# Kernel optimization log

Measured on AMD Instinct MI355X. Metric: run time of the kernel, lower is better.

The kernel has to match this reference:

```python
import jax, jax.numpy as jnp
import numpy as np
from jax import lax

B, C_IN, H, W = 4, 256, 64, 64
C_OUT = 512
KEY_DIM = C_OUT // 2   # 256
VAL_DIM = C_OUT // 2   # 256
HEADS = 8
EPS = 1e-5


def _conv(x, w, stride, pad):
    return lax.conv_general_dilated(
        x, w, (stride, stride), [(pad, pad), (pad, pad)],
        dimension_numbers=('NCHW', 'OIHW', 'NCHW'))


def setup_inputs() -> dict:
    key = jax.random.key(0)
    ks = jax.random.split(key, 10)
    x = jax.random.normal(ks[0], (B, C_IN, H, W), jnp.float32)
    bn_gamma = jax.random.uniform(ks[1], (C_IN,), jnp.float32, 0.5, 1.5)
    bn_beta = jax.random.normal(ks[2], (C_IN,), jnp.float32) * 0.1
    bn_mean = jax.random.normal(ks[3], (C_IN,), jnp.float32) * 0.1
    bn_var = jax.random.uniform(ks[4], (C_IN,), jnp.float32, 0.5, 1.5)
    w_short = jax.random.normal(ks[5], (C_OUT, C_IN, 3, 3), jnp.float32) * (1.0 / np.sqrt(C_IN * 9))
    wq = jax.random.normal(ks[6], (KEY_DIM, C_IN, 1, 1), jnp.float32) * (1.0 / np.sqrt(C_IN))
    wk = jax.random.normal(ks[7], (KEY_DIM, C_IN, 1, 1), jnp.float32) * (1.0 / np.sqrt(C_IN))
    wv = jax.random.normal(ks[8], (VAL_DIM, C_IN, 1, 1), jnp.float32) * (1.0 / np.sqrt(C_IN))
    wo = jax.random.normal(ks[9], (C_OUT, VAL_DIM, 1, 1), jnp.float32) * (1.0 / np.sqrt(VAL_DIM))
    return dict(x=x, bn_gamma=bn_gamma, bn_beta=bn_beta, bn_mean=bn_mean,
                bn_var=bn_var, w_short=w_short, wq=wq, wk=wk, wv=wv, wo=wo)


def reference(x, bn_gamma, bn_beta, bn_mean, bn_var, w_short, wq, wk, wv, wo):
    # BatchNorm (inference: running stats) + ReLU, fused elementwise chain
    inv = bn_gamma / jnp.sqrt(bn_var + EPS)
    h = jax.nn.relu((x - bn_mean[None, :, None, None]) * inv[None, :, None, None]
                    + bn_beta[None, :, None, None])

    # Projection shortcut: 3x3 conv, stride 2, pad 1, no bias -> [B, C_OUT, H/2, W/2]
    shortcut = _conv(h, w_short, 2, 1)

    # DOWN attention: queries at stride 2 (downsampled grid), keys/values at full res
    q = _conv(h, wq, 2, 0)   # [B, KEY_DIM, H/2, W/2]
    k = _conv(h, wk, 1, 0)   # [B, KEY_DIM, H, W]
    v = _conv(h, wv, 1, 0)   # [B, VAL_DIM, H, W]

    Ho, Wo = H // 2, W // 2
    dk = KEY_DIM // HEADS
    dv = VAL_DIM // HEADS
    Nq, Nk = Ho * Wo, H * W

    qh = q.reshape(B, HEADS, dk, Nq)
    kh = k.reshape(B, HEADS, dk, Nk)
    vh = v.reshape(B, HEADS, dv, Nk)

    scale = 1.0 / np.sqrt(dk)
    scores = jnp.einsum('bhdq,bhdk->bhqk', qh, kh) * scale  # [B,H,Nq,Nk]
    attn = jax.nn.softmax(scores, axis=-1)                  # use_softmax=True
    out = jnp.einsum('bhqk,bhdk->bhdq', attn, vh)           # [B,H,dv,Nq]
    out = out.reshape(B, VAL_DIM, Ho, Wo)
    out = _conv(out, wo, 1, 0)                              # [B, C_OUT, Ho, Wo]

    return shortcut + out
```

## Files before the change

kernel.cpp:

```cpp
#include <hip/hip_runtime.h>

#define BB    4
#define CIN   256
#define NPIX  4096
#define COUT  512
#define KD    256
#define HEADS 8
#define NQ    1024
#define NK    4096
#define EPSV  1e-5f
#define QSCALE (0.17677669529663687f * 1.4426950408889634f)

using short8 = __attribute__((ext_vector_type(8))) short;
using f32x4  = __attribute__((ext_vector_type(4))) float;

__device__ __forceinline__ float b2f(unsigned u){ return __uint_as_float(u << 16); }
__device__ __forceinline__ unsigned short f2b(float f){
  unsigned u = __float_as_uint(f);
  return (unsigned short)((u + 0x7fffu + ((u >> 16) & 1u)) >> 16);
}
__device__ __forceinline__ float bnrelu(float xv, float inv, float mu, float bt){
  return fmaxf((xv - mu) * inv + bt, 0.0f);
}
__device__ __forceinline__ unsigned pkbf(float lo, float hi){
  unsigned a = __float_as_uint(lo) + 0x8000u;
  unsigned b = __float_as_uint(hi) + 0x8000u;
  return __builtin_amdgcn_perm(b, a, 0x07060302u);
}
__device__ __forceinline__ unsigned cvtpk(float lo, float hi){
  unsigned r;
  asm("v_cvt_pk_bf16_f32 %0, %1, %2" : "=v"(r) : "v"(lo), "v"(hi));
  return r;
}

#define WF_K  2560
#define WF_E  (512*2560)

__global__ __launch_bounds__(256) void prep_all(
    const float* __restrict__ x, const float* __restrict__ gam,
    const float* __restrict__ bet, const float* __restrict__ mea,
    const float* __restrict__ var,
    const float* __restrict__ wsh, const float* __restrict__ wq,
    const float* __restrict__ wk,  const float* __restrict__ wv,
    const float* __restrict__ wo,
    unsigned short* __restrict__ h_t, unsigned short* __restrict__ W2){
  __shared__ unsigned short T[64][264];
  const int blk = blockIdx.x;
  const int t = threadIdx.x;
  if (blk < 832){
    if (blk < 512){
      float* R = (float*)&T[0][0];
      const float* src = wsh + (size_t)blk * 2304;
      #pragma unroll
      for (int i = 0; i < 9; ++i) R[i * 256 + t] = src[i * 256 + t];
      __syncthreads();
      unsigned short* dst = W2 + (size_t)blk * WF_K;
      #pragma unroll
      for (int i = 0; i < 9; ++i){
        int kp = i * 256 + t;
        int tap = kp >> 8, ci = kp & 255;
        dst[kp] = f2b(R[ci * 9 + tap]);
      }
    } else if (blk < 704){
      int idx = (blk - 512) * 1024 + t * 4;
      float4 v;
      if (idx < 65536){
        v = *(const float4*)(wq + idx);
        v.x *= QSCALE; v.y *= QSCALE; v.z *= QSCALE; v.w *= QSCALE;
      } else if (idx < 2*65536){ v = *(const float4*)(wk + idx - 65536);
      } else {                   v = *(const float4*)(wv + idx - 2*65536); }
      uint2 pk;
      pk.x = (unsigned)f2b(v.x) | ((unsigned)f2b(v.y) << 16);
      pk.y = (unsigned)f2b(v.z) | ((unsigned)f2b(v.w) << 16);
      *(uint2*)(W2 + WF_E + idx) = pk;
    } else {
      int idx = (blk - 704) * 1024 + t * 4;
      int m = idx >> 8, c = idx & 255;
      float4 v = *(const float4*)(wo + idx);
      uint2 pk;
      pk.x = (unsigned)f2b(v.x) | ((unsigned)f2b(v.y) << 16);
      pk.y = (unsigned)f2b(v.z) | ((unsigned)f2b(v.w) << 16);
      *(uint2*)(W2 + (size_t)m * WF_K + 2304 + c) = pk;
    }
    return;
  }
  const int lin = blk - 832;
  const int b = lin >> 6;
  const int pix0 = (lin & 63) * 64;
  const int w = t >> 6, lane = t & 63;
  for (int cc = 0; cc < 32; ++cc){
    int c0 = cc * 8 + w * 2;
    float i0 = gam[c0]   * rsqrtf(var[c0]   + EPSV), mu0 = mea[c0],   bt0 = bet[c0];
    float i1 = gam[c0+1] * rsqrtf(var[c0+1] + EPSV), mu1 = mea[c0+1], bt1 = bet[c0+1];
    float v0 = bnrelu(x[((size_t)(b*CIN + c0  ))*NPIX + pix0 + lane], i0, mu0, bt0);
    float v1 = bnrelu(x[((size_t)(b*CIN + c0+1))*NPIX + pix0 + lane], i1, mu1, bt1);
    *(unsigned*)&T[lane][c0] = pkbf(v0, v1);
  }
  __syncthreads();
  int p = t >> 2;
  unsigned short* dst = h_t + ((size_t)b * NPIX + pix0 + p) * CIN;
  #pragma unroll
  for (int i = 0; i < 8; ++i){
    int coff = i * 32 + (t & 3) * 8;
    *(uint4*)(dst + coff) = *(const uint4*)&T[p][coff];
  }
}

__global__ __launch_bounds__(256) void qkv_gemm(
    const unsigned short* __restrict__ Wkv,
    const unsigned short* __restrict__ Wq,
    const unsigned short* __restrict__ h_t,
    unsigned short* __restrict__ ktg,
    unsigned short* __restrict__ vtg,
    unsigned short* __restrict__ qt){
  __shared__ unsigned short As[64][72];
  __shared__ unsigned short Bs[128][72];
  const int b = blockIdx.z;
  const int t = threadIdx.x;
  const int w = t >> 6, lane = t & 63, col = lane & 15, quad = lane >> 4;
  const int wm = w & 1, wn = w >> 1;

  if (blockIdx.y < 8){
    const int m0 = blockIdx.y * 64;
    const bool isv = m0 >= 256;
    const int n0 = blockIdx.x * 128;
    f32x4 acc[2][4];
    #pragma unroll
    for (int i = 0; i < 2; ++i)
      #pragma unroll
      for (int j = 0; j < 4; ++j) acc[i][j] = (f32x4){0.f,0.f,0.f,0.f};
    const int am = t >> 2, ak = (t & 3) * 8;
    const int bn = t >> 1, bkh = (t & 1) * 16;
    const size_t browbase = ((size_t)b * NPIX + (n0 + bn)) * CIN;

    uint4 av0 = *(const uint4*)(Wkv + (size_t)(m0 + am) * 256 + ak);
    uint4 av1 = *(const uint4*)(Wkv + (size_t)(m0 + am) * 256 + 32 + ak);
    uint4 bv0 = *(const uint4*)(h_t + browbase + bkh);
    uint4 bv1 = *(const uint4*)(h_t + browbase + bkh + 8);
    uint4 bv2 = *(const uint4*)(h_t + browbase + 32 + bkh);
    uint4 bv3 = *(const uint4*)(h_t + browbase + 32 + bkh + 8);

    for (int k0 = 0; k0 < 256; k0 += 64){
      *(uint4*)&As[am][ak]           = av0;
      *(uint4*)&As[am][32 + ak]      = av1;
      *(uint4*)&Bs[bn][bkh]          = bv0;
      *(uint4*)&Bs[bn][bkh + 8]      = bv1;
      *(uint4*)&Bs[bn][32 + bkh]     = bv2;
      *(uint4*)&Bs[bn][32 + bkh + 8] = bv3;
      __syncthreads();
      if (k0 + 64 < 256){
        av0 = *(const uint4*)(Wkv + (size_t)(m0 + am) * 256 + k0 + 64 + ak);
        av1 = *(const uint4*)(Wkv + (size_t)(m0 + am) * 256 + k0 + 96 + ak);
        bv0 = *(const uint4*)(h_t + browbase + k0 + 64 + bkh);
        bv1 = *(const uint4*)(h_t + browbase + k0 + 64 + bkh + 8);
        bv2 = *(const uint4*)(h_t + browbase + k0 + 96 + bkh);
        bv3 = *(const uint4*)(h_t + browbase + k0 + 96 + bkh + 8);
      }
      #pragma unroll
      for (int h = 0; h < 2; ++h){
        short8 af[2], bf[4];
        af[0] = *(const short8*)&As[wm * 32 +      col][h * 32 + quad * 8];
        af[1] = *(const short8*)&As[wm * 32 + 16 + col][h * 32 + quad * 8];
        #pragma unroll
        for (int j = 0; j < 4; ++j)
          bf[j] = *(const short8*)&Bs[wn * 64 + j * 16 + col][h * 32 + quad * 8];
        if (!isv){
          #pragma unroll
          for (int i = 0; i < 2; ++i)
            #pragma unroll
            for (int j = 0; j < 4; ++j)
              acc[i][j] = __builtin_amdgcn_mfma_f32_16x16x32_bf16(af[i], bf[j], acc[i][j], 0, 0, 0);
        } else {
          #pragma unroll
          for (int i = 0; i < 2; ++i)
            #pragma unroll
            for (int j = 0; j < 4; ++j)
              acc[i][j] = __builtin_amdgcn_mfma_f32_16x16x32_bf16(bf[j], af[i], acc[i][j], 0, 0, 0);
        }
      }
      __syncthreads();
    }

    if (!isv){
      int head = (m0 + wm * 32) >> 5;
      #pragma unroll
      for (int i = 0; i < 2; ++i){
        int d0 = i * 16 + quad * 4;
        #pragma unroll
        for (int j = 0; j < 4; ++j){
          int n = n0 + wn * 64 + j * 16 + col;
          uint2 pk;
          pk.x = pkbf(acc[i][j][0], acc[i][j][1]);
          pk.y = pkbf(acc[i][j][2], acc[i][j][3]);
          *(uint2*)(ktg + ((size_t)(b * HEADS + head) * NK + n) * 32 + d0) = pk;
        }
      }
    } else {
      int head = ((m0 - 256) + wm * 32) >> 5;
      #pragma unroll
      for (int i = 0; i < 2; ++i){
        int d = i * 16 + col;
        #pragma unroll
        for (int j = 0; j < 4; ++j){
          int nb = n0 + wn * 64 + j * 16 + quad * 4;
          size_t addr = (((size_t)(b * HEADS + head) * 128 + (nb >> 5)) * 32 + d) * 32 + (nb & 31);
          uint2 pk;
          pk.x = pkbf(acc[i][j][0], acc[i][j][1]);
          pk.y = pkbf(acc[i][j][2], acc[i][j][3]);
          *(uint2*)(vtg + addr) = pk;
        }
      }
    }
    return;
  }

  const int lin = (blockIdx.y - 8) * 32 + blockIdx.x;
  const int m0 = (lin >> 4) * 64;
  const int n0 = (lin & 15) * 64;
  f32x4 acc[2][2];
  #pragma unroll
  for (int i = 0; i < 2; ++i)
    #pragma unroll
    for (int j = 0; j < 2; ++j) acc[i][j] = (f32x4){0.f,0.f,0.f,0.f};
  const int am = t >> 2, ak = (t & 3) * 8;
  const int bn = t >> 2, bk = (t & 3) * 8;
  int n = n0 + bn;
  const size_t browbase = ((size_t)b * NPIX + (((n >> 5) << 7) + ((n & 31) << 1))) * CIN;

  uint4 av0 = *(const uint4*)(Wq + (size_t)(m0 + am) * 256 + ak);
  uint4 av1 = *(const uint4*)(Wq + (size_t)(m0 + am) * 256 + 32 + ak);
  uint4 bv0 = *(const uint4*)(h_t + browbase + bk);
  uint4 bv1 = *(const uint4*)(h_t + browbase + 32 + bk);

  for (int k0 = 0; k0 < 256; k0 += 64){
    *(uint4*)&As[am][ak]      = av0;
    *(uint4*)&As[am][32 + ak] = av1;
    *(uint4*)&Bs[bn][bk]      = bv0;
    *(uint4*)&Bs[bn][32 + bk] = bv1;
    __syncthreads();
    if (k0 + 64 < 256){
      av0 = *(const uint4*)(Wq + (size_t)(m0 + am) * 256 + k0 + 64 + ak);
      av1 = *(const uint4*)(Wq + (size_t)(m0 + am) * 256 + k0 + 96 + ak);
      bv0 = *(const uint4*)(h_t + browbase + k0 + 64 + bk);
      bv1 = *(const uint4*)(h_t + browbase + k0 + 96 + bk);
    }
    #pragma unroll
    for (int h = 0; h < 2; ++h){
      short8 af[2], bf[2];
      af[0] = *(const short8*)&As[wm * 32 +      col][h * 32 + quad * 8];
      af[1] = *(const short8*)&As[wm * 32 + 16 + col][h * 32 + quad * 8];
      bf[0] = *(const short8*)&Bs[wn * 32 +      col][h * 32 + quad * 8];
      bf[1] = *(const short8*)&Bs[wn * 32 + 16 + col][h * 32 + quad * 8];
      #pragma unroll
      for (int i = 0; i < 2; ++i)
        #pragma unroll
        for (int j = 0; j < 2; ++j)
          acc[i][j] = __builtin_amdgcn_mfma_f32_16x16x32_bf16(af[i], bf[j], acc[i][j], 0, 0, 0);
    }
    __syncthreads();
  }

  int head = (m0 + wm * 32) >> 5;
  #pragma unroll
  for (int i = 0; i < 2; ++i){
    int d0 = i * 16 + quad * 4;
    #pragma unroll
    for (int j = 0; j < 2; ++j){
      int nn = n0 + wn * 32 + j * 16 + col;
      uint2 pk;
      pk.x = pkbf(acc[i][j][0], acc[i][j][1]);
      pk.y = pkbf(acc[i][j][2], acc[i][j][3]);
      *(uint2*)(qt + ((size_t)(b * HEADS + head) * NQ + nn) * 32 + d0) = pk;
    }
  }
}

__global__ __launch_bounds__(256) void scwo_gemm(
    const unsigned short* __restrict__ Wf,
    const unsigned short* __restrict__ h_t,
    const unsigned short* __restrict__ aot,
    float* __restrict__ outf){
  const int b  = blockIdx.z;
  const int m0 = blockIdx.y * 64;
  const int n0 = blockIdx.x * 64;
  const int t  = threadIdx.x;
  const int w = t >> 6, lane = t & 63, col = lane & 15, quad = lane >> 4;
  const int wm = w & 1, wn = w >> 1;
  __shared__ unsigned short As[64][72];
  __shared__ unsigned short Bs[64][72];
  f32x4 acc[2][2];
  #pragma unroll
  for (int i = 0; i < 2; ++i)
    #pragma unroll
    for (int j = 0; j < 2; ++j) acc[i][j] = (f32x4){0.f,0.f,0.f,0.f};
  const int am = t >> 2, ak = (t & 3) * 8;
  const int bn = t >> 2, bk = (t & 3) * 8;
  const int n = n0 + bn;
  const int oy = n >> 5, ox = n & 31;
  const size_t aobase = ((size_t)b * NQ + n) * KD;

  auto loadB = [&](int k0) -> uint4 {
    if (k0 < 2304){
      int tap = k0 >> 8;
      int ky = tap / 3, kx = tap - ky * 3;
      int iy = 2 * oy + ky - 1, ix = 2 * ox + kx - 1;
      if (((unsigned)iy < 64u) && ((unsigned)ix < 64u))
        return *(const uint4*)(h_t + ((size_t)b * NPIX + iy * 64 + ix) * CIN + (k0 & 255) + bk);
      return make_uint4(0,0,0,0);
    }
    return *(const uint4*)(aot + aobase + (k0 - 2304) + bk);
  };

  uint4 av0 = *(const uint4*)(Wf + (size_t)(m0 + am) * WF_K + ak);
  uint4 av1 = *(const uint4*)(Wf + (size_t)(m0 + am) * WF_K + 32 + ak);
  uint4 bv0 = loadB(0);
  uint4 bv1 = loadB(32);

  for (int k0 = 0; k0 < WF_K; k0 += 64){
    *(uint4*)&As[am][ak]      = av0;
    *(uint4*)&As[am][32 + ak] = av1;
    *(uint4*)&Bs[bn][bk]      = bv0;
    *(uint4*)&Bs[bn][32 + bk] = bv1;
    __syncthreads();
    if (k0 + 64 < WF_K){
      av0 = *(const uint4*)(Wf + (size_t)(m0 + am) * WF_K + k0 + 64 + ak);
      av1 = *(const uint4*)(Wf + (size_t)(m0 + am) * WF_K + k0 + 96 + ak);
      bv0 = loadB(k0 + 64);
      bv1 = loadB(k0 + 96);
    }
    #pragma unroll
    for (int h = 0; h < 2; ++h){
      short8 af[2], bf[2];
      af[0] = *(const short8*)&As[wm * 32 +      col][h * 32 + quad * 8];
      af[1] = *(const short8*)&As[wm * 32 + 16 + col][h * 32 + quad * 8];
      bf[0] = *(const short8*)&Bs[wn * 32 +      col][h * 32 + quad * 8];
      bf[1] = *(const short8*)&Bs[wn * 32 + 16 + col][h * 32 + quad * 8];
      #pragma unroll
      for (int i = 0; i < 2; ++i)
        #pragma unroll
        for (int j = 0; j < 2; ++j)
          acc[i][j] = __builtin_amdgcn_mfma_f32_16x16x32_bf16(bf[j], af[i], acc[i][j], 0, 0, 0);
    }
    __syncthreads();
  }

  #pragma unroll
  for (int i = 0; i < 2; ++i){
    int co = m0 + wm * 32 + i * 16 + col;
    #pragma unroll
    for (int j = 0; j < 2; ++j){
      int nb = n0 + wn * 32 + j * 16 + quad * 4;
      float4 o;
      o.x = acc[i][j][0]; o.y = acc[i][j][1];
      o.z = acc[i][j][2]; o.w = acc[i][j][3];
      *(float4*)(outf + ((size_t)(b * COUT + co)) * NQ + nb) = o;
    }
  }
}

__global__ __launch_bounds__(512) void attn9c(
    const unsigned short* __restrict__ qt,
    const unsigned short* __restrict__ ktg,
    const unsigned short* __restrict__ vtg,
    unsigned short* __restrict__ aot){
  __shared__ unsigned short KV[2][8192];
  const int bid = blockIdx.x;
  const int xcd = bid & 7, idx = bid >> 3;
  const int bh = xcd * 4 + (idx & 3);
  const int qg = idx >> 2;
  const int b = bh >> 3, hd = bh & 7;
  const int t = threadIdx.x;
  const int w = t >> 6, lane = t & 63, col = lane & 15, quad = lane >> 4;
  const int q = (qg * 8 + w) * 16 + col;

  short8 qf = *(const short8*)(qt + ((size_t)bh * NQ + q) * 32 + quad * 8);
  const unsigned short* kb = ktg + (size_t)bh * NK * 32;
  const unsigned short* vb = vtg + (size_t)bh * 128 * 1024;

  const int sg = (w & 3) >> 1, sf = w & 1;
  const size_t ksrc = (size_t)(32 * sg + 16 * sf + col) * 32 + quad * 8;
  const size_t vsrc = (size_t)sg * 1024 + (size_t)(16 * sf + col) * 32 + quad * 8;
  const unsigned short* sb = (w < 4) ? kb + ksrc : vb + vsrc;
  unsigned short* ddst = &KV[0][w * 512 + lane * 8 + ((w < 4) ? 0 : 2048)];

  f32x4 O0 = {0.f,0.f,0.f,0.f}, O1 = {0.f,0.f,0.f,0.f}, l4 = {0.f,0.f,0.f,0.f};
  const short8 ones = {0x3F80,0x3F80,0x3F80,0x3F80,0x3F80,0x3F80,0x3F80,0x3F80};

  *(uint4*)ddst          = *(const uint4*)sb;
  *(uint4*)(ddst + 2048) = *(const uint4*)(sb + 2048);
  __syncthreads();

  for (int s = 0; s < 32; ++s){
    const int cur = s & 1;
    uint4 n1, n2;
    if (s + 1 < 32){
      size_t soff = (size_t)(s + 1) * 4096;
      n1 = *(const uint4*)(sb + soff);
      n2 = *(const uint4*)(sb + soff + 2048);
    }
    #pragma unroll
    for (int g = 0; g < 4; ++g){
      const unsigned short* Kp = &KV[cur][g * 1024];
      short8 kf0 = *(const short8*)(Kp +       lane * 8);
      short8 kf1 = *(const short8*)(Kp + 512 + lane * 8);
      f32x4 z = {0.f,0.f,0.f,0.f};
      f32x4 slo = __builtin_amdgcn_mfma_f32_16x16x32_bf16(kf0, qf, z, 0, 0, 0);
      f32x4 shi = __builtin_amdgcn_mfma_f32_16x16x32_bf16(kf1, qf, z, 0, 0, 0);

      unsigned x0 = cvtpk(__builtin_amdgcn_exp2f(slo[0]), __builtin_amdgcn_exp2f(slo[1]));
      unsigned x1 = cvtpk(__builtin_amdgcn_exp2f(slo[2]), __builtin_amdgcn_exp2f(slo[3]));
      unsigned y0 = cvtpk(__builtin_amdgcn_exp2f(shi[0]), __builtin_amdgcn_exp2f(shi[1]));
      unsigned y1 = cvtpk(__builtin_amdgcn_exp2f(shi[2]), __builtin_amdgcn_exp2f(shi[3]));
      asm("v_permlane32_swap_b32 %0, %1" : "+v"(x0), "+v"(y0));
      asm("v_permlane32_swap_b32 %0, %1" : "+v"(x1), "+v"(y1));
      asm("v_permlane16_swap_b32 %0, %1" : "+v"(x0), "+v"(y0));
      asm("v_permlane16_swap_b32 %0, %1" : "+v"(x1), "+v"(y1));
      unsigned f[4] = {x0, x1, y0, y1};
      short8 pf;
      memcpy(&pf, f, 16);

      const unsigned short* Vp = &KV[cur][4096 + g * 1024];
      short8 vf0 = *(const short8*)(Vp +       lane * 8);
      short8 vf1 = *(const short8*)(Vp + 512 + lane * 8);
      O0 = __builtin_amdgcn_mfma_f32_16x16x32_bf16(vf0, pf, O0, 0, 0, 0);
      O1 = __builtin_amdgcn_mfma_f32_16x16x32_bf16(vf1, pf, O1, 0, 0, 0);
      l4 = __builtin_amdgcn_mfma_f32_16x16x32_bf16(ones, pf, l4, 0, 0, 0);
    }
    if (s + 1 < 32){
      *(uint4*)(ddst + (size_t)(cur ^ 1) * 8192)        = n1;
      *(uint4*)(ddst + 2048 + (size_t)(cur ^ 1) * 8192) = n2;
    }
    __syncthreads();
  }

  float inv = 1.0f / l4[0];
  unsigned short* dst = aot + ((size_t)(b * NQ + q)) * KD + hd * 32;
  uint2 pk;
  pk.x = pkbf(O0[0] * inv, O0[1] * inv);
  pk.y = pkbf(O0[2] * inv, O0[3] * inv);
  *(uint2*)(dst + quad * 4) = pk;
  pk.x = pkbf(O1[0] * inv, O1[1] * inv);
  pk.y = pkbf(O1[2] * inv, O1[3] * inv);
  *(uint2*)(dst + 16 + quad * 4) = pk;
}

extern "C" void kernel_launch(void* const* d_in, const int* in_sizes, int n_in,
                              void* d_out, int out_size, void* d_ws, size_t ws_size,
                              hipStream_t stream){
  const float* x   = (const float*)d_in[0];
  const float* bg  = (const float*)d_in[1];
  const float* bbt = (const float*)d_in[2];
  const float* bm  = (const float*)d_in[3];
  const float* bv  = (const float*)d_in[4];
  const float* wsh = (const float*)d_in[5];
  const float* wq  = (const float*)d_in[6];
  const float* wk  = (const float*)d_in[7];
  const float* wvv = (const float*)d_in[8];
  const float* wo  = (const float*)d_in[9];
  float* out = (float*)d_out;

  unsigned short* h_t = (unsigned short*)d_ws;
  unsigned short* W2  = h_t + (size_t)BB * NPIX * CIN;
  unsigned short* qt  = W2  + (WF_E + 3*65536);
  unsigned short* aot = qt  + (size_t)BB * HEADS * NQ * 32;
  unsigned short* ktg = aot + (size_t)BB * NQ * KD;
  unsigned short* vtg = ktg + (size_t)BB * HEADS * NK * 32;
  size_t need = ((size_t)(vtg + (size_t)BB * HEADS * 32 * NK - h_t)) * 2;
  if (ws_size < need) return;

  unsigned short* Wf   = W2;
  unsigned short* wq2  = W2 + WF_E;
  unsigned short* wkv2 = wq2 + 65536;

  prep_all<<<dim3(1088), dim3(256), 0, stream>>>(x, bg, bbt, bm, bv,
                                                 wsh, wq, wk, wvv, wo, h_t, W2);
  qkv_gemm<<<dim3(32, 10, 4), dim3(256), 0, stream>>>(wkv2, wq2, h_t, ktg, vtg, qt);
  attn9c<<<dim3(256), dim3(512), 0, stream>>>(qt, ktg, vtg, aot);
  scwo_gemm<<<dim3(16, 8, 4), dim3(256), 0, stream>>>(Wf, h_t, aot, out);
}
```

Baseline: 166.8 us.

## Split attention key range across wave halves, two query tiles per wave

Each wave now handles two 16-query tiles over half of the key sequence instead of one tile over all of it. This reuses each K/V LDS fragment load for two queries, halving LDS reads per MFMA. The two key-halves are then merged through shared memory at the end, which adds a reduction step, an extra barrier and more accumulator registers. The per-stage K/V staging layout changes so that each half of the block loads its own key range.

```diff
diff --git a/kernel.cpp b/kernel.cpp
--- a/kernel.cpp
+++ b/kernel.cpp
@@ -358,7 +358,7 @@
   }
 }
 
-__global__ __launch_bounds__(512) void attn9c(
+__global__ __launch_bounds__(512) void attn11(
     const unsigned short* __restrict__ qt,
     const unsigned short* __restrict__ ktg,
     const unsigned short* __restrict__ vtg,
@@ -371,9 +371,12 @@
   const int b = bh >> 3, hd = bh & 7;
   const int t = threadIdx.x;
   const int w = t >> 6, lane = t & 63, col = lane & 15, quad = lane >> 4;
-  const int q = (qg * 8 + w) * 16 + col;
-
-  short8 qf = *(const short8*)(qt + ((size_t)bh * NQ + q) * 32 + quad * 8);
+  const int p = w & 3, kh = w >> 2;
+  const int qA = (qg * 8 + 2 * p) * 16 + col;
+  const int qB = qA + 16;
+
+  short8 qfA = *(const short8*)(qt + ((size_t)bh * NQ + qA) * 32 + quad * 8);
+  short8 qfB = *(const short8*)(qt + ((size_t)bh * NQ + qB) * 32 + quad * 8);
   const unsigned short* kb = ktg + (size_t)bh * NK * 32;
   const unsigned short* vb = vtg + (size_t)bh * 128 * 1024;
 
@@ -381,67 +384,112 @@
   const size_t ksrc = (size_t)(32 * sg + 16 * sf + col) * 32 + quad * 8;
   const size_t vsrc = (size_t)sg * 1024 + (size_t)(16 * sf + col) * 32 + quad * 8;
   const unsigned short* sb = (w < 4) ? kb + ksrc : vb + vsrc;
-  unsigned short* ddst = &KV[0][w * 512 + lane * 8 + ((w < 4) ? 0 : 2048)];
-
-  f32x4 O0 = {0.f,0.f,0.f,0.f}, O1 = {0.f,0.f,0.f,0.f}, l4 = {0.f,0.f,0.f,0.f};
+  unsigned short* ddst = &KV[0][w * 512 + lane * 8];
+
+  f32x4 OA0 = {0.f,0.f,0.f,0.f}, OA1 = {0.f,0.f,0.f,0.f}, lA = {0.f,0.f,0.f,0.f};
+  f32x4 OB0 = {0.f,0.f,0.f,0.f}, OB1 = {0.f,0.f,0.f,0.f}, lB = {0.f,0.f,0.f,0.f};
   const short8 ones = {0x3F80,0x3F80,0x3F80,0x3F80,0x3F80,0x3F80,0x3F80,0x3F80};
 
   *(uint4*)ddst          = *(const uint4*)sb;
-  *(uint4*)(ddst + 2048) = *(const uint4*)(sb + 2048);
+  *(uint4*)(ddst + 4096) = *(const uint4*)(sb + 65536);
   __syncthreads();
 
   for (int s = 0; s < 32; ++s){
     const int cur = s & 1;
     uint4 n1, n2;
     if (s + 1 < 32){
-      size_t soff = (size_t)(s + 1) * 4096;
+      size_t soff = (size_t)(s + 1) * 2048;
       n1 = *(const uint4*)(sb + soff);
-      n2 = *(const uint4*)(sb + soff + 2048);
-    }
-    #pragma unroll
-    for (int g = 0; g < 4; ++g){
-      const unsigned short* Kp = &KV[cur][g * 1024];
+      n2 = *(const uint4*)(sb + soff + 65536);
+    }
+    #pragma unroll
+    for (int g = 0; g < 2; ++g){
+      const unsigned short* Kp = &KV[cur][kh * 4096 + g * 1024];
       short8 kf0 = *(const short8*)(Kp +       lane * 8);
       short8 kf1 = *(const short8*)(Kp + 512 + lane * 8);
       f32x4 z = {0.f,0.f,0.f,0.f};
-      f32x4 slo = __builtin_amdgcn_mfma_f32_16x16x32_bf16(kf0, qf, z, 0, 0, 0);
-      f32x4 shi = __builtin_amdgcn_mfma_f32_16x16x32_bf16(kf1, qf, z, 0, 0, 0);
-
-      unsigned x0 = cvtpk(__builtin_amdgcn_exp2f(slo[0]), __builtin_amdgcn_exp2f(slo[1]));
-      unsigned x1 = cvtpk(__builtin_amdgcn_exp2f(slo[2]), __builtin_amdgcn_exp2f(slo[3]));
-      unsigned y0 = cvtpk(__builtin_amdgcn_exp2f(shi[0]), __builtin_amdgcn_exp2f(shi[1]));
-      unsigned y1 = cvtpk(__builtin_amdgcn_exp2f(shi[2]), __builtin_amdgcn_exp2f(shi[3]));
-      asm("v_permlane32_swap_b32 %0, %1" : "+v"(x0), "+v"(y0));
-      asm("v_permlane32_swap_b32 %0, %1" : "+v"(x1), "+v"(y1));
-      asm("v_permlane16_swap_b32 %0, %1" : "+v"(x0), "+v"(y0));
-      asm("v_permlane16_swap_b32 %0, %1" : "+v"(x1), "+v"(y1));
-      unsigned f[4] = {x0, x1, y0, y1};
-      short8 pf;
-      memcpy(&pf, f, 16);
-
-      const unsigned short* Vp = &KV[cur][4096 + g * 1024];
+      f32x4 sloA = __builtin_amdgcn_mfma_f32_16x16x32_bf16(kf0, qfA, z, 0, 0, 0);
+      f32x4 shiA = __builtin_amdgcn_mfma_f32_16x16x32_bf16(kf1, qfA, z, 0, 0, 0);
+      f32x4 sloB = __builtin_amdgcn_mfma_f32_16x16x32_bf16(kf0, qfB, z, 0, 0, 0);
+      f32x4 shiB = __builtin_amdgcn_mfma_f32_16x16x32_bf16(kf1, qfB, z, 0, 0, 0);
+
+      unsigned xa0 = cvtpk(__builtin_amdgcn_exp2f(sloA[0]), __builtin_amdgcn_exp2f(sloA[1]));
+      unsigned xa1 = cvtpk(__builtin_amdgcn_exp2f(sloA[2]), __builtin_amdgcn_exp2f(sloA[3]));
+      unsigned ya0 = cvtpk(__builtin_amdgcn_exp2f(shiA[0]), __builtin_amdgcn_exp2f(shiA[1]));
+      unsigned ya1 = cvtpk(__builtin_amdgcn_exp2f(shiA[2]), __builtin_amdgcn_exp2f(shiA[3]));
+      asm("v_permlane32_swap_b32 %0, %1" : "+v"(xa0), "+v"(ya0));
+      asm("v_permlane32_swap_b32 %0, %1" : "+v"(xa1), "+v"(ya1));
+      asm("v_permlane16_swap_b32 %0, %1" : "+v"(xa0), "+v"(ya0));
+      asm("v_permlane16_swap_b32 %0, %1" : "+v"(xa1), "+v"(ya1));
+      unsigned fa[4] = {xa0, xa1, ya0, ya1};
+      short8 pfA;
+      memcpy(&pfA, fa, 16);
+
+      unsigned xb0 = cvtpk(__builtin_amdgcn_exp2f(sloB[0]), __builtin_amdgcn_exp2f(sloB[1]));
+      unsigned xb1 = cvtpk(__builtin_amdgcn_exp2f(sloB[2]), __builtin_amdgcn_exp2f(sloB[3]));
+      unsigned yb0 = cvtpk(__builtin_amdgcn_exp2f(shiB[0]), __builtin_amdgcn_exp2f(shiB[1]));
+      unsigned yb1 = cvtpk(__builtin_amdgcn_exp2f(shiB[2]), __builtin_amdgcn_exp2f(shiB[3]));
+      asm("v_permlane32_swap_b32 %0, %1" : "+v"(xb0), "+v"(yb0));
+      asm("v_permlane32_swap_b32 %0, %1" : "+v"(xb1), "+v"(yb1));
+      asm("v_permlane16_swap_b32 %0, %1" : "+v"(xb0), "+v"(yb0));
+      asm("v_permlane16_swap_b32 %0, %1" : "+v"(xb1), "+v"(yb1));
+      unsigned fb[4] = {xb0, xb1, yb0, yb1};
+      short8 pfB;
+      memcpy(&pfB, fb, 16);
+
+      const unsigned short* Vp = &KV[cur][kh * 4096 + 2048 + g * 1024];
       short8 vf0 = *(const short8*)(Vp +       lane * 8);
       short8 vf1 = *(const short8*)(Vp + 512 + lane * 8);
-      O0 = __builtin_amdgcn_mfma_f32_16x16x32_bf16(vf0, pf, O0, 0, 0, 0);
-      O1 = __builtin_amdgcn_mfma_f32_16x16x32_bf16(vf1, pf, O1, 0, 0, 0);
-      l4 = __builtin_amdgcn_mfma_f32_16x16x32_bf16(ones, pf, l4, 0, 0, 0);
+      OA0 = __builtin_amdgcn_mfma_f32_16x16x32_bf16(vf0, pfA, OA0, 0, 0, 0);
+      OA1 = __builtin_amdgcn_mfma_f32_16x16x32_bf16(vf1, pfA, OA1, 0, 0, 0);
+      lA  = __builtin_amdgcn_mfma_f32_16x16x32_bf16(ones, pfA, lA, 0, 0, 0);
+      OB0 = __builtin_amdgcn_mfma_f32_16x16x32_bf16(vf0, pfB, OB0, 0, 0, 0);
+      OB1 = __builtin_amdgcn_mfma_f32_16x16x32_bf16(vf1, pfB, OB1, 0, 0, 0);
+      lB  = __builtin_amdgcn_mfma_f32_16x16x32_bf16(ones, pfB, lB, 0, 0, 0);
     }
     if (s + 1 < 32){
       *(uint4*)(ddst + (size_t)(cur ^ 1) * 8192)        = n1;
-      *(uint4*)(ddst + 2048 + (size_t)(cur ^ 1) * 8192) = n2;
+      *(uint4*)(ddst + 4096 + (size_t)(cur ^ 1) * 8192) = n2;
     }
     __syncthreads();
   }
 
-  float inv = 1.0f / l4[0];
-  unsigned short* dst = aot + ((size_t)(b * NQ + q)) * KD + hd * 32;
-  uint2 pk;
-  pk.x = pkbf(O0[0] * inv, O0[1] * inv);
-  pk.y = pkbf(O0[2] * inv, O0[3] * inv);
-  *(uint2*)(dst + quad * 4) = pk;
-  pk.x = pkbf(O1[0] * inv, O1[1] * inv);
-  pk.y = pkbf(O1[2] * inv, O1[3] * inv);
-  *(uint2*)(dst + 16 + quad * 4) = pk;
+  float* M = (float*)&KV[0][0];
+  if (kh == 1){
+    float* dst = M + ((size_t)p * 64 + lane) * 24;
+    *(f32x4*)(dst +  0) = OA0;
+    *(f32x4*)(dst +  4) = OA1;
+    *(f32x4*)(dst +  8) = OB0;
+    *(f32x4*)(dst + 12) = OB1;
+    dst[16] = lA[0];
+    dst[17] = lB[0];
+  }
+  __syncthreads();
+  if (kh == 0){
+    const float* src = M + ((size_t)p * 64 + lane) * 24;
+    {
+      float inv = 1.0f / (lA[0] + src[16]);
+      unsigned short* dst = aot + ((size_t)(b * NQ + qA)) * KD + hd * 32;
+      uint2 pk;
+      pk.x = pkbf((OA0[0] + src[0]) * inv, (OA0[1] + src[1]) * inv);
+      pk.y = pkbf((OA0[2] + src[2]) * inv, (OA0[3] + src[3]) * inv);
+      *(uint2*)(dst + quad * 4) = pk;
+      pk.x = pkbf((OA1[0] + src[4]) * inv, (OA1[1] + src[5]) * inv);
+      pk.y = pkbf((OA1[2] + src[6]) * inv, (OA1[3] + src[7]) * inv);
+      *(uint2*)(dst + 16 + quad * 4) = pk;
+    }
+    {
+      float inv = 1.0f / (lB[0] + src[17]);
+      unsigned short* dst = aot + ((size_t)(b * NQ + qB)) * KD + hd * 32;
+      uint2 pk;
+      pk.x = pkbf((OB0[0] + src[8])  * inv, (OB0[1] + src[9])  * inv);
+      pk.y = pkbf((OB0[2] + src[10]) * inv, (OB0[3] + src[11]) * inv);
+      *(uint2*)(dst + quad * 4) = pk;
+      pk.x = pkbf((OB1[0] + src[12]) * inv, (OB1[1] + src[13]) * inv);
+      pk.y = pkbf((OB1[2] + src[14]) * inv, (OB1[3] + src[15]) * inv);
+      *(uint2*)(dst + 16 + quad * 4) = pk;
+    }
+  }
 }
 
 extern "C" void kernel_launch(void* const* d_in, const int* in_sizes, int n_in,
@@ -475,6 +523,6 @@
   prep_all<<<dim3(1088), dim3(256), 0, stream>>>(x, bg, bbt, bm, bv,
                                                  wsh, wq, wk, wvv, wo, h_t, W2);
   qkv_gemm<<<dim3(32, 10, 4), dim3(256), 0, stream>>>(wkv2, wq2, h_t, ktg, vtg, qt);
-  attn9c<<<dim3(256), dim3(512), 0, stream>>>(qt, ktg, vtg, aot);
+  attn11<<<dim3(256), dim3(512), 0, stream>>>(qt, ktg, vtg, aot);
   scwo_gemm<<<dim3(16, 8, 4), dim3(256), 0, stream>>>(Wf, h_t, aot, out);
 }
```

Result: no change. 170.0 us (+1.9%).

## Split attention over key halves and merge partial results in a separate kernel

Applied to the files above, without the earlier changes.

The attention kernel now splits the key/value range into two halves, so the launch grows from 256 to 512 blocks and each block runs 16 stages instead of 32. Unnormalized fp32 partial outputs and row sums go to workspace, and a new merge kernel adds the two halves, normalizes and writes bf16. The aim is better occupancy across the CUs, since 256 blocks of 512 threads may underfill a 256-CU device. The cost is an extra launch plus fp32 partial traffic. Skipping max subtraction (the exp is unshifted) keeps the plain sum merge valid.

```diff
diff --git a/kernel.cpp b/kernel.cpp
--- a/kernel.cpp
+++ b/kernel.cpp
@@ -358,17 +358,18 @@
   }
 }
 
-__global__ __launch_bounds__(512) void attn9c(
+__global__ __launch_bounds__(512) void attn12(
     const unsigned short* __restrict__ qt,
     const unsigned short* __restrict__ ktg,
     const unsigned short* __restrict__ vtg,
-    unsigned short* __restrict__ aot){
+    float* __restrict__ po,
+    float* __restrict__ pl){
   __shared__ unsigned short KV[2][8192];
   const int bid = blockIdx.x;
   const int xcd = bid & 7, idx = bid >> 3;
   const int bh = xcd * 4 + (idx & 3);
-  const int qg = idx >> 2;
-  const int b = bh >> 3, hd = bh & 7;
+  const int qg = (idx >> 2) & 7;
+  const int kh = idx >> 5;
   const int t = threadIdx.x;
   const int w = t >> 6, lane = t & 63, col = lane & 15, quad = lane >> 4;
   const int q = (qg * 8 + w) * 16 + col;
@@ -380,7 +381,7 @@
   const int sg = (w & 3) >> 1, sf = w & 1;
   const size_t ksrc = (size_t)(32 * sg + 16 * sf + col) * 32 + quad * 8;
   const size_t vsrc = (size_t)sg * 1024 + (size_t)(16 * sf + col) * 32 + quad * 8;
-  const unsigned short* sb = (w < 4) ? kb + ksrc : vb + vsrc;
+  const unsigned short* sb = ((w < 4) ? kb + ksrc : vb + vsrc) + (size_t)kh * 65536;
   unsigned short* ddst = &KV[0][w * 512 + lane * 8 + ((w < 4) ? 0 : 2048)];
 
   f32x4 O0 = {0.f,0.f,0.f,0.f}, O1 = {0.f,0.f,0.f,0.f}, l4 = {0.f,0.f,0.f,0.f};
@@ -390,10 +391,10 @@
   *(uint4*)(ddst + 2048) = *(const uint4*)(sb + 2048);
   __syncthreads();
 
-  for (int s = 0; s < 32; ++s){
+  for (int s = 0; s < 16; ++s){
     const int cur = s & 1;
     uint4 n1, n2;
-    if (s + 1 < 32){
+    if (s + 1 < 16){
       size_t soff = (size_t)(s + 1) * 4096;
       n1 = *(const uint4*)(sb + soff);
       n2 = *(const uint4*)(sb + soff + 2048);
@@ -426,22 +427,48 @@
       O1 = __builtin_amdgcn_mfma_f32_16x16x32_bf16(vf1, pf, O1, 0, 0, 0);
       l4 = __builtin_amdgcn_mfma_f32_16x16x32_bf16(ones, pf, l4, 0, 0, 0);
     }
-    if (s + 1 < 32){
+    if (s + 1 < 16){
       *(uint4*)(ddst + (size_t)(cur ^ 1) * 8192)        = n1;
       *(uint4*)(ddst + 2048 + (size_t)(cur ^ 1) * 8192) = n2;
     }
     __syncthreads();
   }
 
-  float inv = 1.0f / l4[0];
-  unsigned short* dst = aot + ((size_t)(b * NQ + q)) * KD + hd * 32;
-  uint2 pk;
-  pk.x = pkbf(O0[0] * inv, O0[1] * inv);
-  pk.y = pkbf(O0[2] * inv, O0[3] * inv);
-  *(uint2*)(dst + quad * 4) = pk;
-  pk.x = pkbf(O1[0] * inv, O1[1] * inv);
-  pk.y = pkbf(O1[2] * inv, O1[3] * inv);
-  *(uint2*)(dst + 16 + quad * 4) = pk;
+  float* pob = po + (((size_t)(kh * 32 + bh) * NQ + q) * 32);
+  *(f32x4*)(pob + quad * 4)      = O0;
+  *(f32x4*)(pob + 16 + quad * 4) = O1;
+  if (quad == 0) pl[(size_t)(kh * 32 + bh) * NQ + q] = l4[0];
+}
+
+__global__ __launch_bounds__(256) void attn_merge(
+    const float* __restrict__ po, const float* __restrict__ pl,
+    unsigned short* __restrict__ aot){
+  const int g = blockIdx.x * 256 + threadIdx.x;
+  const int pair = g >> 1, half = g & 1;
+  const int bh = pair >> 10, q = pair & 1023;
+  const int b = bh >> 3, hd = bh & 7;
+  const float* p0 = po + ((size_t)bh * NQ + q) * 32 + half * 16;
+  const float* p1 = p0 + (size_t)32 * NQ * 32;
+  float l = pl[(size_t)bh * NQ + q] + pl[(size_t)(32 + bh) * NQ + q];
+  float inv = 1.0f / l;
+  float o[16];
+  #pragma unroll
+  for (int i = 0; i < 16; i += 4){
+    float4 a = *(const float4*)(p0 + i);
+    float4 c = *(const float4*)(p1 + i);
+    o[i]   = (a.x + c.x) * inv;
+    o[i+1] = (a.y + c.y) * inv;
+    o[i+2] = (a.z + c.z) * inv;
+    o[i+3] = (a.w + c.w) * inv;
+  }
+  unsigned short* dst = aot + ((size_t)(b * NQ + q)) * KD + hd * 32 + half * 16;
+  uint4 pk;
+  pk.x = pkbf(o[0],  o[1]);  pk.y = pkbf(o[2],  o[3]);
+  pk.z = pkbf(o[4],  o[5]);  pk.w = pkbf(o[6],  o[7]);
+  *(uint4*)dst = pk;
+  pk.x = pkbf(o[8],  o[9]);  pk.y = pkbf(o[10], o[11]);
+  pk.z = pkbf(o[12], o[13]); pk.w = pkbf(o[14], o[15]);
+  *(uint4*)(dst + 8) = pk;
 }
 
 extern "C" void kernel_launch(void* const* d_in, const int* in_sizes, int n_in,
@@ -465,7 +492,11 @@
   unsigned short* aot = qt  + (size_t)BB * HEADS * NQ * 32;
   unsigned short* ktg = aot + (size_t)BB * NQ * KD;
   unsigned short* vtg = ktg + (size_t)BB * HEADS * NK * 32;
-  size_t need = ((size_t)(vtg + (size_t)BB * HEADS * 32 * NK - h_t)) * 2;
+  unsigned short* wend = vtg + (size_t)BB * HEADS * 32 * NK;
+  float* po = (float*)wend;
+  float* pl = po + (size_t)2 * 32 * NQ * 32;
+  size_t need = ((size_t)(wend - h_t)) * 2
+              + ((size_t)2 * 32 * NQ * 32 + (size_t)2 * 32 * NQ) * 4;
   if (ws_size < need) return;
 
   unsigned short* Wf   = W2;
@@ -475,6 +506,7 @@
   prep_all<<<dim3(1088), dim3(256), 0, stream>>>(x, bg, bbt, bm, bv,
                                                  wsh, wq, wk, wvv, wo, h_t, W2);
   qkv_gemm<<<dim3(32, 10, 4), dim3(256), 0, stream>>>(wkv2, wq2, h_t, ktg, vtg, qt);
-  attn9c<<<dim3(256), dim3(512), 0, stream>>>(qt, ktg, vtg, aot);
+  attn12<<<dim3(512), dim3(512), 0, stream>>>(qt, ktg, vtg, po, pl);
+  attn_merge<<<dim3(256), dim3(256), 0, stream>>>(po, pl, aot);
   scwo_gemm<<<dim3(16, 8, 4), dim3(256), 0, stream>>>(Wf, h_t, aot, out);
 }
```

Result: no change. 165.0 us (median of 3 runs) (-1.1%).
